# Kernel tuning notes

Hardware: AMD Instinct MI355X
Metric: run time of the kernel (lower is better)

## Reference

```python
import jax, jax.numpy as jnp
import numpy as np

B, N_TOK, DIM = 4, 16384, 256
NH, NP = 8, 4
HD = DIM // NH  # 32


def setup_inputs() -> dict:
    key = jax.random.key(0)
    ks = jax.random.split(key, 6)
    s = 0.02
    x = jax.random.normal(ks[0], (B, N_TOK, DIM), jnp.float32)
    v_w = jax.random.normal(ks[1], (DIM, DIM), jnp.float32) * s
    v_b = jnp.zeros((DIM,), jnp.float32)
    aw_w = jax.random.normal(ks[2], (NH * NP, DIM), jnp.float32) * s
    aw_b = jnp.zeros((NH * NP,), jnp.float32)
    # offsets: weight init to zeros, bias init per _reset_parameters
    off_w = jnp.zeros((NH * NP * 2, DIM), jnp.float32)
    thetas = np.arange(NH, dtype=np.float64) * (2.0 * np.pi / NH)
    g = np.stack([np.cos(thetas), np.sin(thetas)], -1)
    g = g / np.abs(g).max(-1, keepdims=True)
    g = np.tile(g[:, None, :], (1, NP, 1)) * np.arange(1, NP + 1)[None, :, None]
    off_b = jnp.asarray(g.reshape(-1), jnp.float32)
    proj_w = jax.random.normal(ks[3], (DIM, DIM), jnp.float32) * s
    proj_b = jnp.zeros((DIM,), jnp.float32)
    return dict(x=x, v_w=v_w, v_b=v_b, aw_w=aw_w, aw_b=aw_b,
                off_w=off_w, off_b=off_b, proj_w=proj_w, proj_b=proj_b,
                H=128, W=128)


def _grad_scale(t, scale):
    sg = jax.lax.stop_gradient(t)
    return sg + scale * (t - sg)


def _bilinear_point_attn(v, grid, weight):
    # v: [G, H, W, D] feature maps; grid: [G, N, P, 2] pixel coords (x, y);
    # weight: [G, N, P]. Zero padding outside the map (MSDeformAttn-style).
    G, Hh, Ww, D = v.shape
    gx, gy = grid[..., 0], grid[..., 1]
    x0 = jnp.floor(gx); y0 = jnp.floor(gy)
    wx1 = gx - x0; wx0 = 1.0 - wx1
    wy1 = gy - y0; wy0 = 1.0 - wy1
    x0i = x0.astype(jnp.int32); y0i = y0.astype(jnp.int32)
    v_flat = v.reshape(G, Hh * Ww, D)

    def gather(xi, yi):
        valid = ((xi >= 0) & (xi < Ww) & (yi >= 0) & (yi < Hh))
        xi_c = jnp.clip(xi, 0, Ww - 1)
        yi_c = jnp.clip(yi, 0, Hh - 1)
        idx = (yi_c * Ww + xi_c).reshape(G, -1, 1)
        g = jnp.take_along_axis(v_flat, idx, axis=1).reshape(*xi.shape, D)
        return g * valid[..., None].astype(v.dtype)

    g00 = gather(x0i, y0i)
    g10 = gather(x0i + 1, y0i)
    g01 = gather(x0i, y0i + 1)
    g11 = gather(x0i + 1, y0i + 1)
    samp = ((wy0 * wx0)[..., None] * g00 + (wy0 * wx1)[..., None] * g10
            + (wy1 * wx0)[..., None] * g01 + (wy1 * wx1)[..., None] * g11)
    # softmax-weighted aggregation over points
    return jnp.einsum('gnpd,gnp->gnd', samp, weight)


def reference(x, v_w, v_b, aw_w, aw_b, off_w, off_b, proj_w, proj_b, H, W):
    Bb, N, C = x.shape
    # v projection -> per-head feature maps [B*nh, H, W, hd]
    v = (x @ v_w.T + v_b).reshape(Bb, N, NH, HD)
    v = v.transpose(0, 2, 1, 3).reshape(Bb * NH, H, W, HD)
    # reference points: (x=col, y=row) pixel coords, shape [1, N, 1, 2]
    mh, mw = jnp.meshgrid(jnp.arange(H, dtype=x.dtype), jnp.arange(W, dtype=x.dtype), indexing='ij')
    ref_points = jnp.stack([mw, mh], -1).reshape(1, N, 1, 2)
    # offsets [B*nh, N, P, 2]
    offsets = (x @ off_w.T + off_b).reshape(Bb, N, NH, NP, 2)
    offsets = offsets.transpose(0, 2, 1, 3, 4).reshape(Bb * NH, N, NP, 2)
    grid = _grad_scale(ref_points + offsets, 0.1)
    # attention weights [B*nh, N, P], softmax over points
    w = (x @ aw_w.T + aw_b).reshape(Bb, N, NH, NP)
    w = w.transpose(0, 2, 1, 3).reshape(Bb * NH, N, NP)
    w = jax.nn.softmax(w, axis=-1)
    out = _bilinear_point_attn(v, grid, w)  # [B*nh, N, hd]
    out = out.reshape(Bb, NH, N, HD).transpose(0, 2, 1, 3).reshape(Bb, N, C)
    return out @ proj_w.T + proj_b
```

## Files before the change

### kernel.cpp

```cpp
#include <hip/hip_runtime.h>


typedef __attribute__((ext_vector_type(8))) short bf16x8;
typedef __attribute__((ext_vector_type(4))) float f32x4;

__device__ __forceinline__ short f2bf(float f) {
  unsigned u = __float_as_uint(f);
  u = u + 0x7FFFu + ((u >> 16) & 1u);
  return (short)(u >> 16);
}

__device__ __forceinline__ void gload16(const void* g, void* l) {
  __builtin_amdgcn_global_load_lds(
      (const __attribute__((address_space(1))) unsigned int*)g,
      (__attribute__((address_space(3))) unsigned int*)l, 16, 0, 0);
}

__global__ __launch_bounds__(256) void k_prep(
    const float* __restrict__ v_w, const float* __restrict__ aw_w,
    const float* __restrict__ off_w, const float* __restrict__ proj_w,
    short* __restrict__ wcat, short* __restrict__ wproj)
{
  int idx = blockIdx.x * 256 + threadIdx.x;
  if (idx < 384 * 256) {
    int row = idx >> 8;
    float val = 0.f;
    if (row < 256)      val = v_w[idx];
    else if (row < 288) val = aw_w[idx - 256 * 256];
    else if (row < 352) val = off_w[idx - 288 * 256];
    wcat[idx] = f2bf(val);
  } else {
    int j = idx - 384 * 256;
    wproj[j] = f2bf(proj_w[j]);
  }
}

__global__ __launch_bounds__(256) void k_proj(
    const float* __restrict__ x, const short* __restrict__ wcat,
    const float* __restrict__ v_b, const float* __restrict__ aw_b,
    const float* __restrict__ off_b,
    float* __restrict__ vbuf,
    float* __restrict__ awraw,
    float* __restrict__ offraw)
{
  __shared__ short As[128 * 64];
  __shared__ short Bs[128 * 64];
  const int tid  = threadIdx.x;
  const int wave = tid >> 6, lane = tid & 63;
  const int c0   = blockIdx.x << 7;
  const int row0 = blockIdx.y << 7;

  const int ar  = tid >> 1;
  const int acb = (tid & 1) << 5;
  const float* xg = x + (size_t)(row0 + ar) * 256 + acb;

  const int wr = wave >> 1, wc = wave & 1;
  const int lr = lane & 15, kg = lane >> 4;

  f32x4 acc[4][4] = {};

  for (int kt = 0; kt < 4; ++kt) {
#pragma unroll
    for (int i = 0; i < 4; ++i) {
      int fb = ((wave << 2) + i) << 6;
      int f  = fb + lane;
      int r  = f >> 3, s = f & 7;
      int g  = s ^ (r & 7);
      const short* src = wcat + (size_t)(c0 + r) * 256 + (kt << 6) + (g << 3);
      gload16(src, &Bs[(size_t)fb << 3]);
    }
    {
      const float* ap = xg + (kt << 6);
      f32x4 fv[8];
#pragma unroll
      for (int i = 0; i < 8; ++i) fv[i] = ((const f32x4*)ap)[i];
#pragma unroll
      for (int i = 0; i < 4; ++i) {
        bf16x8 v;
#pragma unroll
        for (int j = 0; j < 4; ++j) { v[j] = f2bf(fv[2*i][j]); v[4+j] = f2bf(fv[2*i+1][j]); }
        int g = ((tid & 1) << 2) + i;
        int s = g ^ (ar & 7);
        *(bf16x8*)&As[(ar << 6) + (s << 3)] = v;
      }
    }
    __syncthreads();

#pragma unroll
    for (int ks = 0; ks < 2; ++ks) {
      bf16x8 a[4], b[4];
#pragma unroll
      for (int m = 0; m < 4; ++m) {
        int r = (wr << 6) + (m << 4) + lr;
        int g = (ks << 2) + kg;
        a[m] = *(const bf16x8*)&As[(r << 6) + ((g ^ (r & 7)) << 3)];
      }
#pragma unroll
      for (int n = 0; n < 4; ++n) {
        int r = (wc << 6) + (n << 4) + lr;
        int g = (ks << 2) + kg;
        b[n] = *(const bf16x8*)&Bs[(r << 6) + ((g ^ (r & 7)) << 3)];
      }
#pragma unroll
      for (int m = 0; m < 4; ++m)
#pragma unroll
        for (int n = 0; n < 4; ++n)
          acc[m][n] = __builtin_amdgcn_mfma_f32_16x16x32_bf16(a[m], b[n], acc[m][n], 0, 0, 0);
    }
    __syncthreads();
  }

#pragma unroll
  for (int m = 0; m < 4; ++m) {
#pragma unroll
    for (int n = 0; n < 4; ++n) {
#pragma unroll
      for (int j = 0; j < 4; ++j) {
        int r = row0 + (wr << 6) + (m << 4) + ((lane >> 4) << 2) + j;
        int c = c0 + (wc << 6) + (n << 4) + lr;
        float v = acc[m][n][j];
        int b_ = r >> 14, nn = r & 16383;
        if (c < 256) {
          float val = v + v_b[c];
          int h = c >> 5, d = c & 31;
          vbuf[((((size_t)((b_ << 3) + h)) << 14) + nn) * 32 + d] = val;
        } else if (c < 288) {
          int q = c - 256;
          int h = q >> 2, p = q & 3;
          awraw[((((size_t)((b_ << 3) + h)) << 14) + nn) * 4 + p] = v + aw_b[q];
        } else if (c < 352) {
          int q = c - 288;
          int h = q >> 3, rest = q & 7;
          offraw[((((size_t)((b_ << 3) + h)) << 14) + nn) * 8 + rest] = v + off_b[q];
        }
      }
    }
  }
}

__global__ __launch_bounds__(256) void k_sample(
    const float* __restrict__ vbuf, const float* __restrict__ awraw,
    const float* __restrict__ offraw, unsigned short* __restrict__ attn)
{
  const int tid  = threadIdx.x;
  const int item = (blockIdx.x << 5) + (tid >> 3);
  const int q    = tid & 7;
  const int g = item >> 14, n = item & 16383;
  const float px = (float)(n & 127), py = (float)(n >> 7);

  f32x4 aw = *(const f32x4*)(awraw + (size_t)item * 4);
  const f32x4* opv = (const f32x4*)(offraw + (size_t)item * 8);
  f32x4 o0 = opv[0], o1 = opv[1];

  float mx = fmaxf(fmaxf(aw[0], aw[1]), fmaxf(aw[2], aw[3]));
  float e0 = __expf(aw[0] - mx), e1 = __expf(aw[1] - mx);
  float e2 = __expf(aw[2] - mx), e3 = __expf(aw[3] - mx);
  float inv = __fdividef(1.f, e0 + e1 + e2 + e3);
  float wts[4] = {e0 * inv, e1 * inv, e2 * inv, e3 * inv};
  float oxs[4] = {o0[0], o0[2], o1[0], o1[2]};
  float oys[4] = {o0[1], o0[3], o1[1], o1[3]};

  const float* vg = vbuf + (((size_t)g) << 19);
  f32x4 o = {0.f, 0.f, 0.f, 0.f};
#pragma unroll
  for (int p = 0; p < 4; ++p) {
    float gx = px + oxs[p], gy = py + oys[p];
    float x0f = floorf(gx), y0f = floorf(gy);
    float wx1 = gx - x0f, wx0 = 1.f - wx1;
    float wy1 = gy - y0f, wy0 = 1.f - wy1;
    int x0 = (int)x0f, y0 = (int)y0f;
    const float* base = vg + (((y0 << 7) + x0) << 5) + (q << 2);
    bool xv0 = (unsigned)x0 < 128u, xv1 = (unsigned)(x0 + 1) < 128u;
    bool yv0 = (unsigned)y0 < 128u, yv1 = (unsigned)(y0 + 1) < 128u;
    f32x4 c00 = {0,0,0,0}, c10 = {0,0,0,0}, c01 = {0,0,0,0}, c11 = {0,0,0,0};
    if (xv0 & yv0) c00 = *(const f32x4*)(base);
    if (xv1 & yv0) c10 = *(const f32x4*)(base + 32);
    if (xv0 & yv1) c01 = *(const f32x4*)(base + 4096);
    if (xv1 & yv1) c11 = *(const f32x4*)(base + 4128);
    float w00 = wts[p] * (wy0 * wx0), w10 = wts[p] * (wy0 * wx1);
    float w01 = wts[p] * (wy1 * wx0), w11 = wts[p] * (wy1 * wx1);
    o += w00 * c00 + w10 * c10 + w01 * c01 + w11 * c11;
  }
  int b_ = g >> 3, h = g & 7;
  union { unsigned long long u64; unsigned short us[4]; } pk;
#pragma unroll
  for (int j = 0; j < 4; ++j) pk.us[j] = (unsigned short)f2bf(o[j]);
  *(unsigned long long*)(attn + ((((size_t)b_ << 14) + n) << 8) + (h << 5) + (q << 2)) = pk.u64;
}

__global__ __launch_bounds__(256) void k_out(
    const unsigned short* __restrict__ attn, const short* __restrict__ wproj,
    const float* __restrict__ proj_b, float* __restrict__ out)
{
  __shared__ short As[128 * 64];
  __shared__ short Bs[128 * 64];
  const int tid  = threadIdx.x;
  const int wave = tid >> 6, lane = tid & 63;
  const int c0   = blockIdx.x << 7;
  const int row0 = blockIdx.y << 7;

  const int wr = wave >> 1, wc = wave & 1;
  const int lr = lane & 15, kg = lane >> 4;

  f32x4 acc[4][4] = {};

  for (int kt = 0; kt < 4; ++kt) {
#pragma unroll
    for (int i = 0; i < 4; ++i) {
      int fb = ((wave << 2) + i) << 6;
      int f  = fb + lane;
      int r  = f >> 3, s = f & 7;
      int g  = s ^ (r & 7);
      const short* srcA = (const short*)attn + (size_t)(row0 + r) * 256 + (kt << 6) + (g << 3);
      const short* srcB = wproj + (size_t)(c0 + r) * 256 + (kt << 6) + (g << 3);
      gload16(srcA, &As[(size_t)fb << 3]);
      gload16(srcB, &Bs[(size_t)fb << 3]);
    }
    __syncthreads();

#pragma unroll
    for (int ks = 0; ks < 2; ++ks) {
      bf16x8 a[4], b[4];
#pragma unroll
      for (int m = 0; m < 4; ++m) {
        int r = (wr << 6) + (m << 4) + lr;
        int g = (ks << 2) + kg;
        a[m] = *(const bf16x8*)&As[(r << 6) + ((g ^ (r & 7)) << 3)];
      }
#pragma unroll
      for (int n = 0; n < 4; ++n) {
        int r = (wc << 6) + (n << 4) + lr;
        int g = (ks << 2) + kg;
        b[n] = *(const bf16x8*)&Bs[(r << 6) + ((g ^ (r & 7)) << 3)];
      }
#pragma unroll
      for (int m = 0; m < 4; ++m)
#pragma unroll
        for (int n = 0; n < 4; ++n)
          acc[m][n] = __builtin_amdgcn_mfma_f32_16x16x32_bf16(a[m], b[n], acc[m][n], 0, 0, 0);
    }
    __syncthreads();
  }

#pragma unroll
  for (int m = 0; m < 4; ++m) {
#pragma unroll
    for (int n = 0; n < 4; ++n) {
#pragma unroll
      for (int j = 0; j < 4; ++j) {
        int r = row0 + (wr << 6) + (m << 4) + ((lane >> 4) << 2) + j;
        int c = c0 + (wc << 6) + (n << 4) + lr;
        out[(size_t)r * 256 + c] = acc[m][n][j] + proj_b[c];
      }
    }
  }
}

extern "C" void kernel_launch(void* const* d_in, const int* in_sizes, int n_in,
                              void* d_out, int out_size, void* d_ws, size_t ws_size,
                              hipStream_t stream)
{
  const float* x      = (const float*)d_in[0];
  const float* v_w    = (const float*)d_in[1];
  const float* v_b    = (const float*)d_in[2];
  const float* aw_w   = (const float*)d_in[3];
  const float* aw_b   = (const float*)d_in[4];
  const float* off_w  = (const float*)d_in[5];
  const float* off_b  = (const float*)d_in[6];
  const float* proj_w = (const float*)d_in[7];
  const float* proj_b = (const float*)d_in[8];
  float* out = (float*)d_out;

  char* ws = (char*)d_ws;
  short* wcat   = (short*)(ws + 0);
  short* wproj  = (short*)(ws + 262144);
  float* awraw  = (float*)(ws + 1048576);
  float* offraw = (float*)(ws + 9437184);
  unsigned short* attn = (unsigned short*)(ws + 26214400);
  float* vbuf = (float*)d_out;

  hipLaunchKernelGGL(k_prep,   dim3(640),      dim3(256), 0, stream,
                     v_w, aw_w, off_w, proj_w, wcat, wproj);
  hipLaunchKernelGGL(k_proj,   dim3(3, 512),   dim3(256), 0, stream,
                     x, wcat, v_b, aw_b, off_b, vbuf, awraw, offraw);
  hipLaunchKernelGGL(k_sample, dim3(16384),    dim3(256), 0, stream,
                     vbuf, awraw, offraw, attn);
  hipLaunchKernelGGL(k_out,    dim3(2, 512),   dim3(256), 0, stream,
                     attn, wproj, proj_b, out);
}
```

Before: 258.7 us.

## Store value maps in bf16, fuse softmax into projection, widen GEMM tiles

```diff
diff --git a/kernel.cpp b/kernel.cpp
--- a/kernel.cpp
+++ b/kernel.cpp
@@ -8,6 +8,9 @@
   unsigned u = __float_as_uint(f);
   u = u + 0x7FFFu + ((u >> 16) & 1u);
   return (short)(u >> 16);
+}
+__device__ __forceinline__ float bf2f(short s) {
+  return __uint_as_float(((unsigned)(unsigned short)s) << 16);
 }
 
 __device__ __forceinline__ void gload16(const void* g, void* l) {
@@ -39,47 +42,46 @@
     const float* __restrict__ x, const short* __restrict__ wcat,
     const float* __restrict__ v_b, const float* __restrict__ aw_b,
     const float* __restrict__ off_b,
-    float* __restrict__ vbuf,
-    float* __restrict__ awraw,
+    unsigned short* __restrict__ vbuf,
+    float* __restrict__ wts,
     float* __restrict__ offraw)
 {
-  __shared__ short As[128 * 64];
-  __shared__ short Bs[128 * 64];
+  __shared__ short As[64 * 64];
+  __shared__ short Bs[384 * 64];
   const int tid  = threadIdx.x;
   const int wave = tid >> 6, lane = tid & 63;
-  const int c0   = blockIdx.x << 7;
-  const int row0 = blockIdx.y << 7;
-
-  const int ar  = tid >> 1;
-  const int acb = (tid & 1) << 5;
-  const float* xg = x + (size_t)(row0 + ar) * 256 + acb;
-
-  const int wr = wave >> 1, wc = wave & 1;
+  const int row0 = blockIdx.x << 6;
+
+  const int ar  = tid >> 2;
+  const int seg = tid & 3;
+  const float* xg = x + (size_t)(row0 + ar) * 256 + (seg << 4);
+
   const int lr = lane & 15, kg = lane >> 4;
-
-  f32x4 acc[4][4] = {};
+  const int cb = wave * 96;
+
+  f32x4 acc[4][6] = {};
 
   for (int kt = 0; kt < 4; ++kt) {
 #pragma unroll
-    for (int i = 0; i < 4; ++i) {
-      int fb = ((wave << 2) + i) << 6;
+    for (int i = 0; i < 12; ++i) {
+      int fb = (wave * 12 + i) << 6;
       int f  = fb + lane;
       int r  = f >> 3, s = f & 7;
       int g  = s ^ (r & 7);
-      const short* src = wcat + (size_t)(c0 + r) * 256 + (kt << 6) + (g << 3);
+      const short* src = wcat + (size_t)r * 256 + (kt << 6) + (g << 3);
       gload16(src, &Bs[(size_t)fb << 3]);
     }
     {
       const float* ap = xg + (kt << 6);
-      f32x4 fv[8];
-#pragma unroll
-      for (int i = 0; i < 8; ++i) fv[i] = ((const f32x4*)ap)[i];
-#pragma unroll
-      for (int i = 0; i < 4; ++i) {
+      f32x4 fv[4];
+#pragma unroll
+      for (int i = 0; i < 4; ++i) fv[i] = ((const f32x4*)ap)[i];
+#pragma unroll
+      for (int i = 0; i < 2; ++i) {
         bf16x8 v;
 #pragma unroll
         for (int j = 0; j < 4; ++j) { v[j] = f2bf(fv[2*i][j]); v[4+j] = f2bf(fv[2*i+1][j]); }
-        int g = ((tid & 1) << 2) + i;
+        int g = (seg << 1) + i;
         int s = g ^ (ar & 7);
         *(bf16x8*)&As[(ar << 6) + (s << 3)] = v;
       }
@@ -88,50 +90,59 @@
 
 #pragma unroll
     for (int ks = 0; ks < 2; ++ks) {
-      bf16x8 a[4], b[4];
+      bf16x8 a[4], b[6];
 #pragma unroll
       for (int m = 0; m < 4; ++m) {
-        int r = (wr << 6) + (m << 4) + lr;
+        int r = (m << 4) + lr;
         int g = (ks << 2) + kg;
         a[m] = *(const bf16x8*)&As[(r << 6) + ((g ^ (r & 7)) << 3)];
       }
 #pragma unroll
-      for (int n = 0; n < 4; ++n) {
-        int r = (wc << 6) + (n << 4) + lr;
+      for (int n = 0; n < 6; ++n) {
+        int r = cb + (n << 4) + lr;
         int g = (ks << 2) + kg;
         b[n] = *(const bf16x8*)&Bs[(r << 6) + ((g ^ (r & 7)) << 3)];
       }
 #pragma unroll
       for (int m = 0; m < 4; ++m)
 #pragma unroll
-        for (int n = 0; n < 4; ++n)
+        for (int n = 0; n < 6; ++n)
           acc[m][n] = __builtin_amdgcn_mfma_f32_16x16x32_bf16(a[m], b[n], acc[m][n], 0, 0, 0);
     }
     __syncthreads();
   }
 
 #pragma unroll
-  for (int m = 0; m < 4; ++m) {
-#pragma unroll
-    for (int n = 0; n < 4; ++n) {
+  for (int n = 0; n < 6; ++n) {
+    const int cbase = cb + (n << 4);
+    if (cbase >= 352) continue;
+#pragma unroll
+    for (int m = 0; m < 4; ++m) {
 #pragma unroll
       for (int j = 0; j < 4; ++j) {
-        int r = row0 + (wr << 6) + (m << 4) + ((lane >> 4) << 2) + j;
-        int c = c0 + (wc << 6) + (n << 4) + lr;
+        int r = row0 + (m << 4) + (kg << 2) + j;
+        int b_ = r >> 14, nn = r & 16383;
         float v = acc[m][n][j];
-        int b_ = r >> 14, nn = r & 16383;
-        if (c < 256) {
+        if (cbase < 256) {
+          int c = cbase + lr;
+          int h = c >> 5, d = c & 31;
           float val = v + v_b[c];
-          int h = c >> 5, d = c & 31;
-          vbuf[((((size_t)((b_ << 3) + h)) << 14) + nn) * 32 + d] = val;
-        } else if (c < 288) {
-          int q = c - 256;
+          vbuf[(((size_t)((b_ << 3) + h) << 14) + nn) * 32 + d] = (unsigned short)f2bf(val);
+        } else if (cbase < 288) {
+          int q = cbase - 256 + lr;
+          float val = v + aw_b[q];
+          float mx = fmaxf(val, __shfl_xor(val, 1));
+          mx = fmaxf(mx, __shfl_xor(mx, 2));
+          float e = __expf(val - mx);
+          float s = e + __shfl_xor(e, 1);
+          s += __shfl_xor(s, 2);
+          float w = __fdividef(e, s);
           int h = q >> 2, p = q & 3;
-          awraw[((((size_t)((b_ << 3) + h)) << 14) + nn) * 4 + p] = v + aw_b[q];
-        } else if (c < 352) {
-          int q = c - 288;
+          wts[(((size_t)((b_ << 3) + h) << 14) + nn) * 4 + p] = w;
+        } else {
+          int q = cbase - 288 + lr;
           int h = q >> 3, rest = q & 7;
-          offraw[((((size_t)((b_ << 3) + h)) << 14) + nn) * 8 + rest] = v + off_b[q];
+          offraw[(((size_t)((b_ << 3) + h) << 14) + nn) * 8 + rest] = v + off_b[q];
         }
       }
     }
@@ -139,29 +150,24 @@
 }
 
 __global__ __launch_bounds__(256) void k_sample(
-    const float* __restrict__ vbuf, const float* __restrict__ awraw,
+    const unsigned short* __restrict__ vbuf, const float* __restrict__ wts,
     const float* __restrict__ offraw, unsigned short* __restrict__ attn)
 {
   const int tid  = threadIdx.x;
-  const int item = (blockIdx.x << 5) + (tid >> 3);
-  const int q    = tid & 7;
+  const int item = (blockIdx.x << 6) + (tid >> 2);
+  const int q    = tid & 3;
   const int g = item >> 14, n = item & 16383;
   const float px = (float)(n & 127), py = (float)(n >> 7);
 
-  f32x4 aw = *(const f32x4*)(awraw + (size_t)item * 4);
+  f32x4 w4 = *(const f32x4*)(wts + (size_t)item * 4);
   const f32x4* opv = (const f32x4*)(offraw + (size_t)item * 8);
   f32x4 o0 = opv[0], o1 = opv[1];
-
-  float mx = fmaxf(fmaxf(aw[0], aw[1]), fmaxf(aw[2], aw[3]));
-  float e0 = __expf(aw[0] - mx), e1 = __expf(aw[1] - mx);
-  float e2 = __expf(aw[2] - mx), e3 = __expf(aw[3] - mx);
-  float inv = __fdividef(1.f, e0 + e1 + e2 + e3);
-  float wts[4] = {e0 * inv, e1 * inv, e2 * inv, e3 * inv};
+  float wv[4]  = {w4[0], w4[1], w4[2], w4[3]};
   float oxs[4] = {o0[0], o0[2], o1[0], o1[2]};
   float oys[4] = {o0[1], o0[3], o1[1], o1[3]};
 
-  const float* vg = vbuf + (((size_t)g) << 19);
-  f32x4 o = {0.f, 0.f, 0.f, 0.f};
+  const unsigned short* vg = vbuf + (((size_t)g) << 19) + (q << 3);
+  float o[8] = {};
 #pragma unroll
   for (int p = 0; p < 4; ++p) {
     float gx = px + oxs[p], gy = py + oys[p];
@@ -169,51 +175,60 @@
     float wx1 = gx - x0f, wx0 = 1.f - wx1;
     float wy1 = gy - y0f, wy0 = 1.f - wy1;
     int x0 = (int)x0f, y0 = (int)y0f;
-    const float* base = vg + (((y0 << 7) + x0) << 5) + (q << 2);
     bool xv0 = (unsigned)x0 < 128u, xv1 = (unsigned)(x0 + 1) < 128u;
     bool yv0 = (unsigned)y0 < 128u, yv1 = (unsigned)(y0 + 1) < 128u;
-    f32x4 c00 = {0,0,0,0}, c10 = {0,0,0,0}, c01 = {0,0,0,0}, c11 = {0,0,0,0};
-    if (xv0 & yv0) c00 = *(const f32x4*)(base);
-    if (xv1 & yv0) c10 = *(const f32x4*)(base + 32);
-    if (xv0 & yv1) c01 = *(const f32x4*)(base + 4096);
-    if (xv1 & yv1) c11 = *(const f32x4*)(base + 4128);
-    float w00 = wts[p] * (wy0 * wx0), w10 = wts[p] * (wy0 * wx1);
-    float w01 = wts[p] * (wy1 * wx0), w11 = wts[p] * (wy1 * wx1);
-    o += w00 * c00 + w10 * c10 + w01 * c01 + w11 * c11;
+    const unsigned short* base = vg + (((y0 << 7) + x0) << 5);
+    bf16x8 c00 = {}, c10 = {}, c01 = {}, c11 = {};
+    if (xv0 & yv0) c00 = *(const bf16x8*)(base);
+    if (xv1 & yv0) c10 = *(const bf16x8*)(base + 32);
+    if (xv0 & yv1) c01 = *(const bf16x8*)(base + 4096);
+    if (xv1 & yv1) c11 = *(const bf16x8*)(base + 4128);
+    float w00 = wv[p] * (wy0 * wx0), w10 = wv[p] * (wy0 * wx1);
+    float w01 = wv[p] * (wy1 * wx0), w11 = wv[p] * (wy1 * wx1);
+#pragma unroll
+    for (int j = 0; j < 8; ++j)
+      o[j] += w00 * bf2f(c00[j]) + w10 * bf2f(c10[j])
+            + w01 * bf2f(c01[j]) + w11 * bf2f(c11[j]);
   }
   int b_ = g >> 3, h = g & 7;
-  union { unsigned long long u64; unsigned short us[4]; } pk;
-#pragma unroll
-  for (int j = 0; j < 4; ++j) pk.us[j] = (unsigned short)f2bf(o[j]);
-  *(unsigned long long*)(attn + ((((size_t)b_ << 14) + n) << 8) + (h << 5) + (q << 2)) = pk.u64;
-}
-
-__global__ __launch_bounds__(256) void k_out(
+  bf16x8 pk;
+#pragma unroll
+  for (int j = 0; j < 8; ++j) pk[j] = f2bf(o[j]);
+  *(bf16x8*)(attn + ((((size_t)b_ << 14) + n) << 8) + (h << 5) + (q << 3)) = pk;
+}
+
+__global__ __launch_bounds__(512) void k_out(
     const unsigned short* __restrict__ attn, const short* __restrict__ wproj,
     const float* __restrict__ proj_b, float* __restrict__ out)
 {
   __shared__ short As[128 * 64];
-  __shared__ short Bs[128 * 64];
+  __shared__ short Bs[256 * 64];
   const int tid  = threadIdx.x;
   const int wave = tid >> 6, lane = tid & 63;
-  const int c0   = blockIdx.x << 7;
-  const int row0 = blockIdx.y << 7;
-
-  const int wr = wave >> 1, wc = wave & 1;
+  const int row0 = blockIdx.x << 7;
+
+  const int wr = wave >> 2, wc = wave & 3;
   const int lr = lane & 15, kg = lane >> 4;
 
   f32x4 acc[4][4] = {};
 
   for (int kt = 0; kt < 4; ++kt) {
+#pragma unroll
+    for (int i = 0; i < 2; ++i) {
+      int fb = ((wave << 1) + i) << 6;
+      int f  = fb + lane;
+      int r  = f >> 3, s = f & 7;
+      int g  = s ^ (r & 7);
+      const short* srcA = (const short*)attn + (size_t)(row0 + r) * 256 + (kt << 6) + (g << 3);
+      gload16(srcA, &As[(size_t)fb << 3]);
+    }
 #pragma unroll
     for (int i = 0; i < 4; ++i) {
       int fb = ((wave << 2) + i) << 6;
       int f  = fb + lane;
       int r  = f >> 3, s = f & 7;
       int g  = s ^ (r & 7);
-      const short* srcA = (const short*)attn + (size_t)(row0 + r) * 256 + (kt << 6) + (g << 3);
-      const short* srcB = wproj + (size_t)(c0 + r) * 256 + (kt << 6) + (g << 3);
-      gload16(srcA, &As[(size_t)fb << 3]);
+      const short* srcB = wproj + (size_t)r * 256 + (kt << 6) + (g << 3);
       gload16(srcB, &Bs[(size_t)fb << 3]);
     }
     __syncthreads();
@@ -248,8 +263,8 @@
     for (int n = 0; n < 4; ++n) {
 #pragma unroll
       for (int j = 0; j < 4; ++j) {
-        int r = row0 + (wr << 6) + (m << 4) + ((lane >> 4) << 2) + j;
-        int c = c0 + (wc << 6) + (n << 4) + lr;
+        int r = row0 + (wr << 6) + (m << 4) + (kg << 2) + j;
+        int c = (wc << 6) + (n << 4) + lr;
         out[(size_t)r * 256 + c] = acc[m][n][j] + proj_b[c];
       }
     }
@@ -274,17 +289,17 @@
   char* ws = (char*)d_ws;
   short* wcat   = (short*)(ws + 0);
   short* wproj  = (short*)(ws + 262144);
-  float* awraw  = (float*)(ws + 1048576);
+  float* wts    = (float*)(ws + 1048576);
   float* offraw = (float*)(ws + 9437184);
   unsigned short* attn = (unsigned short*)(ws + 26214400);
-  float* vbuf = (float*)d_out;
-
-  hipLaunchKernelGGL(k_prep,   dim3(640),      dim3(256), 0, stream,
+  unsigned short* vbuf = (unsigned short*)d_out;
+
+  hipLaunchKernelGGL(k_prep,   dim3(640),   dim3(256), 0, stream,
                      v_w, aw_w, off_w, proj_w, wcat, wproj);
-  hipLaunchKernelGGL(k_proj,   dim3(3, 512),   dim3(256), 0, stream,
-                     x, wcat, v_b, aw_b, off_b, vbuf, awraw, offraw);
-  hipLaunchKernelGGL(k_sample, dim3(16384),    dim3(256), 0, stream,
-                     vbuf, awraw, offraw, attn);
-  hipLaunchKernelGGL(k_out,    dim3(2, 512),   dim3(256), 0, stream,
+  hipLaunchKernelGGL(k_proj,   dim3(1024),  dim3(256), 0, stream,
+                     x, wcat, v_b, aw_b, off_b, vbuf, wts, offraw);
+  hipLaunchKernelGGL(k_sample, dim3(8192),  dim3(256), 0, stream,
+                     vbuf, wts, offraw, attn);
+  hipLaunchKernelGGL(k_out,    dim3(512),   dim3(512), 0, stream,
                      attn, wproj, proj_b, out);
 }
```

Measured after the change: 282.4 us. 9.2% more time.
